# Kernel tuning notes

Measured on AMD Instinct MI355X. Metric: run time of the kernel, lower is better.

Reference implementation:

```python
import jax, jax.numpy as jnp
import numpy as np

SIGMA1 = 1.0        # RBF bandwidth for kernel1
DYADIC_ORDER = 1    # dyadic grid refinement
LAMBD = 1.0         # ridge regularizer
INPUT_SCALE = 0.1   # keep signature-kernel values in fp32 range


def rbf_gram(X, Y, sigma):
    # X: (N,S,D), Y: (M,T,D) -> (N,M,S,T), sigkernel RBFKernel: exp(-||x-y||^2 / sigma)
    x2 = jnp.sum(X * X, axis=-1)  # (N,S)
    y2 = jnp.sum(Y * Y, axis=-1)  # (M,T)
    xy = jnp.einsum('nsd,mtd->nmst', X, Y)
    d2 = x2[:, None, :, None] + y2[None, :, None, :] - 2.0 * xy
    return jnp.exp(-d2 / sigma)


def linear_gram(X, Y):
    # sigkernel LinearKernel: inner product Gram
    return jnp.einsum('nsd,mtd->nmst', X, Y)


def sig_kernel_gram(G, dyadic_order):
    """Solve the Goursat PDE for the signature kernel on a dyadic grid.

    G: (N,M,S,T) static-kernel Gram. Returns (N,M) signature-kernel Gram.
    Update (sigkernel explicit scheme):
      k[i+1,j+1] = (k[i+1,j] + k[i,j+1]) * (1 + inc/2 + inc^2/12)
                   - k[i,j] * (1 - inc^2/12)
    """
    N, M, S, T = G.shape
    # double increments of the static kernel
    inc = G[:, :, 1:, 1:] - G[:, :, 1:, :-1] - G[:, :, :-1, 1:] + G[:, :, :-1, :-1]
    f = 2 ** dyadic_order
    inc = jnp.repeat(jnp.repeat(inc, f, axis=2), f, axis=3) / float(f * f)
    B = N * M
    P, Q = (S - 1) * f, (T - 1) * f
    inc = inc.reshape(B, P, Q)
    C1 = 1.0 + 0.5 * inc + inc * inc * (1.0 / 12.0)
    C2 = 1.0 - inc * inc * (1.0 / 12.0)
    ones_b = jnp.ones((B,), G.dtype)

    def row_step(prev_row, coeffs):
        c1, c2 = coeffs  # (B,Q) each

        def col_step(left, v):
            c1j, c2j, pj, pjm1 = v  # each (B,)
            new = (left + pj) * c1j - pjm1 * c2j
            return new, new

        xs = (c1.T, c2.T, prev_row[:, 1:].T, prev_row[:, :-1].T)  # (Q,B)
        _, vals = jax.lax.scan(col_step, ones_b, xs)  # (Q,B)
        new_row = jnp.concatenate([ones_b[:, None], vals.T], axis=1)  # (B,Q+1)
        return new_row, None

    row0 = jnp.ones((B, Q + 1), G.dtype)
    last_row, _ = jax.lax.scan(row_step, row0, (jnp.moveaxis(C1, 1, 0), jnp.moveaxis(C2, 1, 0)))
    return last_row[:, -1].reshape(N, M)


def cmmd(x, y, z):
    N = x.shape[0]
    K = sig_kernel_gram(rbf_gram(x, x, SIGMA1), DYADIC_ORDER)
    L_gen = sig_kernel_gram(linear_gram(y, y), DYADIC_ORDER)
    L_true = sig_kernel_gram(linear_gram(z, z), DYADIC_ORDER)
    L_mix = sig_kernel_gram(linear_gram(y, z), DYADIC_ORDER)
    Ktildeinv = jnp.linalg.inv(K + jnp.eye(N, dtype=K.dtype) * LAMBD)
    A = K @ Ktildeinv  # shared left factor

    def tr(L):
        return jnp.trace(A @ (L @ Ktildeinv))

    return tr(L_gen) + tr(L_true) - 2.0 * tr(L_mix)


def setup_inputs() -> dict:
    key = jax.random.key(0)
    k1, k2, k3 = jax.random.split(key, 3)
    shape = (64, 33, 8)
    return {
        'x': jax.random.normal(k1, shape, dtype=jnp.float32) * INPUT_SCALE,
        'y': jax.random.normal(k2, shape, dtype=jnp.float32) * INPUT_SCALE,
        'z': jax.random.normal(k3, shape, dtype=jnp.float32) * INPUT_SCALE,
    }


def reference(x, y, z):
    return cmmd(x, y, z)
```

## Files before the change

kernel.cpp:

```cpp
#include <hip/hip_runtime.h>
#include <hip/hip_fp16.h>
#include <math.h>


#define SLEN 33

__device__ __forceinline__ float rl(float v, int lane) {
    return __int_as_float(__builtin_amdgcn_readlane(__float_as_int(v), lane));
}

__device__ __forceinline__ void pde_item(int g, int loc,
                                         const float* __restrict__ x,
                                         const float* __restrict__ y,
                                         const float* __restrict__ z,
                                         float* __restrict__ ws,
                                         float4 (*Xi4)[66],
                                         __half (*incH)[1024]) {
    const int lane = threadIdx.x & 63;
    const int h = lane >> 5;
    const int p = lane & 31;

    int pair = 2 * loc + h, gi, gj;
    if (g == 3) {
        gi = pair >> 6; gj = pair & 63;
    } else {
        float ff = sqrtf(8.0f * (float)pair + 1.0f);
        gi = (int)((ff - 1.0f) * 0.5f);
        while ((gi + 1) * (gi + 2) / 2 <= pair) ++gi;
        while (gi * (gi + 1) / 2 > pair) --gi;
        gj = pair - gi * (gi + 1) / 2;
    }

    const float* Ap = (g == 0) ? x : ((g == 2) ? z : y);
    const float* Bp = (g == 0) ? x : ((g == 1) ? y : z);
    const float4* As = (const float4*)(Ap + gi * (SLEN * 8));
    const float4* Bs = (const float4*)(Bp + gj * (SLEN * 8));

    for (int k = p; k < 66; k += 32) Xi4[h][k] = As[k];
    float4 b0 = Bs[2*p],   b1 = Bs[2*p+1];
    float4 b2 = Bs[2*p+2], b3 = Bs[2*p+3];
    __syncthreads();

    if (g == 0) {
        float nprev;
        {
            float4 a0 = Xi4[h][0], a1 = Xi4[h][1];
            float d0=a0.x-b0.x,d1=a0.y-b0.y,d2=a0.z-b0.z,d3=a0.w-b0.w;
            float d4=a1.x-b1.x,d5=a1.y-b1.y,d6=a1.z-b1.z,d7=a1.w-b1.w;
            float da = d0*d0+d1*d1+d2*d2+d3*d3+d4*d4+d5*d5+d6*d6+d7*d7;
            float e0=a0.x-b2.x,e1=a0.y-b2.y,e2=a0.z-b2.z,e3=a0.w-b2.w;
            float e4=a1.x-b3.x,e5=a1.y-b3.y,e6=a1.z-b3.z,e7=a1.w-b3.w;
            float db = e0*e0+e1*e1+e2*e2+e3*e3+e4*e4+e5*e5+e6*e6+e7*e7;
            nprev = __expf(-db) - __expf(-da);
        }
        for (int k = 1; k <= 32; ++k) {
            float4 a0 = Xi4[h][2*k], a1 = Xi4[h][2*k+1];
            float d0=a0.x-b0.x,d1=a0.y-b0.y,d2=a0.z-b0.z,d3=a0.w-b0.w;
            float d4=a1.x-b1.x,d5=a1.y-b1.y,d6=a1.z-b1.z,d7=a1.w-b1.w;
            float da = d0*d0+d1*d1+d2*d2+d3*d3+d4*d4+d5*d5+d6*d6+d7*d7;
            float e0=a0.x-b2.x,e1=a0.y-b2.y,e2=a0.z-b2.z,e3=a0.w-b2.w;
            float e4=a1.x-b3.x,e5=a1.y-b3.y,e6=a1.z-b3.z,e7=a1.w-b3.w;
            float db = e0*e0+e1*e1+e2*e2+e3*e3+e4*e4+e5*e5+e6*e6+e7*e7;
            float diffk = __expf(-db) - __expf(-da);
            incH[h][(k-1)*32 + p] = __float2half(0.25f * (diffk - nprev));
            nprev = diffk;
        }
    } else {
        float e0=b2.x-b0.x, e1=b2.y-b0.y, e2=b2.z-b0.z, e3=b2.w-b0.w;
        float e4=b3.x-b1.x, e5=b3.y-b1.y, e6=b3.z-b1.z, e7=b3.w-b1.w;
        float4 a0 = Xi4[h][0], a1 = Xi4[h][1];
        #pragma unroll 4
        for (int k = 0; k < 32; ++k) {
            float4 a2 = Xi4[h][2*k+2], a3 = Xi4[h][2*k+3];
            float acc = (a2.x-a0.x)*e0 + (a2.y-a0.y)*e1
                      + (a2.z-a0.z)*e2 + (a2.w-a0.w)*e3
                      + (a3.x-a1.x)*e4 + (a3.y-a1.y)*e5
                      + (a3.z-a1.z)*e6 + (a3.w-a1.w)*e7;
            incH[h][k*32 + p] = __float2half(0.25f * acc);
            a0 = a2; a1 = a3;
        }
    }
    __syncthreads();

    float c01 = 1.0f, c10 = 1.0f, c11 = 1.0f, dcarry = 1.0f;
    const bool isrow0 = (p == 0);
    const __half* incrow = &incH[h][p * 32];
    #pragma unroll 4
    for (int m = 0; m < 63; ++m) {
        float nb10 = __shfl_up(c10, 1);
        float nb11 = __shfl_up(c11, 1);
        int t = m - p;
        float incv = __half2float(incrow[t & 31]);
        float n0 = isrow0 ? 1.0f : nb10;
        float n1 = isrow0 ? 1.0f : nb11;
        bool t0 = (t == 0);
        float w0 = t0 ? 1.0f : c01;
        float w1 = t0 ? 1.0f : c11;
        float d  = t0 ? 1.0f : dcarry;
        float i2 = incv * incv * (1.0f / 12.0f);
        float C1 = 1.0f + 0.5f * incv + i2;
        float C2 = 1.0f - i2;
        float v00 = (w0  + n0 ) * C1 - d   * C2;
        float v01 = (v00 + n1 ) * C1 - n0  * C2;
        float v10 = (v00 + w1 ) * C1 - w0  * C2;
        float v11 = (v10 + v01) * C1 - v00 * C2;
        c01 = v01; c10 = v10; c11 = v11;
        dcarry = n1;
    }

    if (p == 31) {
        float* dst = ws + g * 4096;
        dst[gi * 64 + gj] = c11;
        if (g != 3) dst[gj * 64 + gi] = c11;
    }
}

__global__ __launch_bounds__(64, 5)
void pdeK_kernel(const float* __restrict__ x, const float* __restrict__ y,
                 const float* __restrict__ z, float* __restrict__ ws) {
    __shared__ float4 XiS[2][66];
    __shared__ __half incS[2][1024];
    pde_item(0, blockIdx.x, x, y, z, ws, XiS, incS);
}

__global__ __launch_bounds__(512, 4)
void pdeL_gj_kernel(const float* __restrict__ x, const float* __restrict__ y,
                    const float* __restrict__ z, float* __restrict__ ws) {
    __shared__ float4 XiS[16][66];
    __shared__ __half incS[16][1024];
    __shared__ float prow[2][2][64];

    const int b   = blockIdx.x;
    const int tid = threadIdx.x;
    const int wv  = tid >> 6;

    if (b == 0) {
        const int c = tid & 63, w = wv;
        const float* K = ws;
        float* Kinv = ws + 16384;
        float m[8];
        #pragma unroll
        for (int i = 0; i < 8; ++i) {
            int r = w * 8 + i;
            m[i] = K[r * 64 + c] + ((r == c) ? 1.0f : 0.0f);
        }
        #pragma unroll 1
        for (int it = 0; it < 8; ++it) {
            #pragma unroll
            for (int j = 0; j < 4; ++j) {
                const int p0 = 8 * it + 2 * j, p1 = p0 + 1;
                const int i0 = 2 * j, i1 = i0 + 1;
                const int buf = j & 1;
                if (w == it) {
                    float x0 = m[i0], x1 = m[i1];
                    float a  = rl(x0, p0), bq = rl(x0, p1);
                    float cq = rl(x1, p0), dq = rl(x1, p1);
                    float dinv = 1.0f / (a * dq - bq * cq);
                    float P00 =  dq * dinv, P01 = -bq * dinv;
                    float P10 = -cq * dinv, P11 =  a  * dinv;
                    float sp0 = P00 * x0 + P01 * x1;
                    float sp1 = P10 * x0 + P11 * x1;
                    sp0 = (c == p0) ? P00 : ((c == p1) ? P01 : sp0);
                    sp1 = (c == p0) ? P10 : ((c == p1) ? P11 : sp1);
                    m[i0] = sp0; m[i1] = sp1;
                    prow[buf][0][c] = sp0;
                    prow[buf][1][c] = sp1;
                }
                __syncthreads();
                float s0  = prow[buf][0][c],  s1  = prow[buf][1][c];
                float q00 = prow[buf][0][p0], q01 = prow[buf][0][p1];
                float q10 = prow[buf][1][p0], q11 = prow[buf][1][p1];
                #pragma unroll
                for (int i = 0; i < 8; ++i) {
                    bool pivotRow = (w == it) && (i == i0 || i == i1);
                    float f0 = rl(m[i], p0);
                    float f1 = rl(m[i], p1);
                    float nv = m[i] - f0 * s0 - f1 * s1;
                    float wb0 = -(f0 * q00 + f1 * q10);
                    float wb1 = -(f0 * q01 + f1 * q11);
                    nv = (c == p0) ? wb0 : ((c == p1) ? wb1 : nv);
                    if (!pivotRow) m[i] = nv;
                }
            }
        }
        #pragma unroll
        for (int i = 0; i < 8; ++i)
            Kinv[(w * 8 + i) * 64 + c] = m[i];
    } else {
        int item = (b - 1) * 8 + wv;
        int g, loc;
        if (item < 1040)      { g = 1; loc = item; }
        else if (item < 2080) { g = 2; loc = item - 1040; }
        else                  { g = 3; loc = item - 2080; }
        pde_item(g, loc, x, y, z, ws, &XiS[2 * wv], &incS[2 * wv]);
        if (b <= 5) {
            int item2 = 4088 + (b - 1) * 8 + wv;
            pde_item(3, item2 - 2080, x, y, z, ws, &XiS[2 * wv], &incS[2 * wv]);
        }
    }
}

__global__ __launch_bounds__(64)
void trace_partial_kernel(const float* __restrict__ ws, float* __restrict__ partial) {
    const int i    = blockIdx.x;
    const int lane = threadIdx.x;
    const float* Lg   = ws + 4096;
    const float* Lt   = ws + 8192;
    const float* Lm   = ws + 12288;
    const float* Kinv = ws + 16384;

    float u = Kinv[i * 64 + lane];
    float acc = 0.0f;
    #pragma unroll 8
    for (int k = 0; k < 64; ++k)
        acc = fmaf(__shfl(u, k), Kinv[k * 64 + lane], acc);
    float wv = u - acc;

    float lc = Lg[lane * 64 + i] + Lt[lane * 64 + i] - 2.0f * Lm[lane * 64 + i];
    float local = wv * lc;
    #pragma unroll
    for (int off = 32; off > 0; off >>= 1)
        local += __shfl_down(local, off);
    if (lane == 0) partial[i] = local;
}

__global__ __launch_bounds__(64)
void final_sum_kernel(const float* __restrict__ partial, float* __restrict__ out) {
    float v = partial[threadIdx.x];
    #pragma unroll
    for (int off = 32; off > 0; off >>= 1)
        v += __shfl_down(v, off);
    if (threadIdx.x == 0) out[0] = v;
}

extern "C" void kernel_launch(void* const* d_in, const int* in_sizes, int n_in,
                              void* d_out, int out_size, void* d_ws, size_t ws_size,
                              hipStream_t stream) {
    const float* x = (const float*)d_in[0];
    const float* y = (const float*)d_in[1];
    const float* z = (const float*)d_in[2];
    float* out = (float*)d_out;
    float* ws  = (float*)d_ws;

    pdeK_kernel<<<1040, 64, 0, stream>>>(x, y, z, ws);
    pdeL_gj_kernel<<<512, 512, 0, stream>>>(x, y, z, ws);
    trace_partial_kernel<<<64, 64, 0, stream>>>(ws, ws + 5 * 4096);
    final_sum_kernel<<<1, 64, 0, stream>>>(ws + 5 * 4096, out);
}
```

Baseline: 100.6 us.

## Fuse trace reduction into PDE/inverse kernel using an atomic completion counter

Result: slower. 103.3 us (+2.7%).

```diff
diff --git a/kernel.cpp b/kernel.cpp
--- a/kernel.cpp
+++ b/kernel.cpp
@@ -124,11 +124,19 @@
 }
 
 __global__ __launch_bounds__(512, 4)
-void pdeL_gj_kernel(const float* __restrict__ x, const float* __restrict__ y,
-                    const float* __restrict__ z, float* __restrict__ ws) {
-    __shared__ float4 XiS[16][66];
-    __shared__ __half incS[16][1024];
+void pdeL_gj_trace_kernel(const float* __restrict__ x,
+                          const float* __restrict__ y,
+                          const float* __restrict__ z,
+                          float* __restrict__ ws,
+                          unsigned int* __restrict__ counter,
+                          float* __restrict__ out) {
+    union U {
+        struct { float4 XiS[16][66]; __half incS[16][1024]; } pde;
+        float Kls[64 * 65];
+    };
+    __shared__ U sm;
     __shared__ float prow[2][2][64];
+    __shared__ float red[8];
 
     const int b   = blockIdx.x;
     const int tid = threadIdx.x;
@@ -137,7 +145,6 @@
     if (b == 0) {
         const int c = tid & 63, w = wv;
         const float* K = ws;
-        float* Kinv = ws + 16384;
         float m[8];
         #pragma unroll
         for (int i = 0; i < 8; ++i) {
@@ -185,52 +192,57 @@
         }
         #pragma unroll
         for (int i = 0; i < 8; ++i)
-            Kinv[(w * 8 + i) * 64 + c] = m[i];
+            sm.Kls[(w * 8 + i) * 65 + c] = m[i];
+
+        if (tid == 0) {
+            while (atomicAdd(counter, 0u) < 516u)
+                __builtin_amdgcn_s_sleep(2);
+        }
+        __syncthreads();
+        __threadfence();
+
+        const float* Lg = ws + 4096;
+        const float* Lt = ws + 8192;
+        const float* Lm = ws + 12288;
+        float acc[8] = {0,0,0,0,0,0,0,0};
+        #pragma unroll 2
+        for (int k = 0; k < 64; ++k) {
+            float rv = sm.Kls[k * 65 + c];
+            #pragma unroll
+            for (int i = 0; i < 8; ++i)
+                acc[i] = fmaf(rl(m[i], k), rv, acc[i]);
+        }
+        float local = 0.0f;
+        #pragma unroll
+        for (int i = 0; i < 8; ++i) {
+            int r = w * 8 + i;
+            float lc = Lg[r * 64 + c] + Lt[r * 64 + c] - 2.0f * Lm[r * 64 + c];
+            local += (m[i] - acc[i]) * lc;
+        }
+        #pragma unroll
+        for (int off = 32; off > 0; off >>= 1)
+            local += __shfl_down(local, off);
+        if (c == 0) red[w] = local;
+        __syncthreads();
+        if (tid == 0) {
+            float v = 0.0f;
+            #pragma unroll
+            for (int i = 0; i < 8; ++i) v += red[i];
+            out[0] = v;
+        }
     } else {
         int item = (b - 1) * 8 + wv;
         int g, loc;
         if (item < 1040)      { g = 1; loc = item; }
         else if (item < 2080) { g = 2; loc = item - 1040; }
         else                  { g = 3; loc = item - 2080; }
-        pde_item(g, loc, x, y, z, ws, &XiS[2 * wv], &incS[2 * wv]);
-        if (b <= 5) {
-            int item2 = 4088 + (b - 1) * 8 + wv;
-            pde_item(3, item2 - 2080, x, y, z, ws, &XiS[2 * wv], &incS[2 * wv]);
-        }
-    }
-}
-
-__global__ __launch_bounds__(64)
-void trace_partial_kernel(const float* __restrict__ ws, float* __restrict__ partial) {
-    const int i    = blockIdx.x;
-    const int lane = threadIdx.x;
-    const float* Lg   = ws + 4096;
-    const float* Lt   = ws + 8192;
-    const float* Lm   = ws + 12288;
-    const float* Kinv = ws + 16384;
-
-    float u = Kinv[i * 64 + lane];
-    float acc = 0.0f;
-    #pragma unroll 8
-    for (int k = 0; k < 64; ++k)
-        acc = fmaf(__shfl(u, k), Kinv[k * 64 + lane], acc);
-    float wv = u - acc;
-
-    float lc = Lg[lane * 64 + i] + Lt[lane * 64 + i] - 2.0f * Lm[lane * 64 + i];
-    float local = wv * lc;
-    #pragma unroll
-    for (int off = 32; off > 0; off >>= 1)
-        local += __shfl_down(local, off);
-    if (lane == 0) partial[i] = local;
-}
-
-__global__ __launch_bounds__(64)
-void final_sum_kernel(const float* __restrict__ partial, float* __restrict__ out) {
-    float v = partial[threadIdx.x];
-    #pragma unroll
-    for (int off = 32; off > 0; off >>= 1)
-        v += __shfl_down(v, off);
-    if (threadIdx.x == 0) out[0] = v;
+        pde_item(g, loc, x, y, z, ws, &sm.pde.XiS[2 * wv], &sm.pde.incS[2 * wv]);
+        __syncthreads();
+        if (tid == 0) {
+            __threadfence();
+            atomicAdd(counter, 1u);
+        }
+    }
 }
 
 extern "C" void kernel_launch(void* const* d_in, const int* in_sizes, int n_in,
@@ -241,9 +253,9 @@
     const float* z = (const float*)d_in[2];
     float* out = (float*)d_out;
     float* ws  = (float*)d_ws;
-
+    unsigned int* counter = (unsigned int*)(ws + 16384);
+
+    hipMemsetAsync(counter, 0, sizeof(unsigned int), stream);
     pdeK_kernel<<<1040, 64, 0, stream>>>(x, y, z, ws);
-    pdeL_gj_kernel<<<512, 512, 0, stream>>>(x, y, z, ws);
-    trace_partial_kernel<<<64, 64, 0, stream>>>(ws, ws + 5 * 4096);
-    final_sum_kernel<<<1, 64, 0, stream>>>(ws + 5 * 4096, out);
-}
+    pdeL_gj_trace_kernel<<<517, 512, 0, stream>>>(x, y, z, ws, counter, out);
+}
```
